# Kernel optimization log

Hardware: AMD Instinct MI355X
Metric: run time of the kernel (lower is better)

## Reference

```python
import jax, jax.numpy as jnp
import numpy as np

FLOAT_MIN = np.float32(np.finfo(np.float32).min)  # torch.finfo().min for float32
K_DIM = 64  # init kwarg, equals head dim of query/key


def setup_inputs() -> dict:
    key = jax.random.key(0)
    k1, k2, k3, k4 = jax.random.split(key, 4)
    B, Lq, Lk, D, Dv = 16, 2048, 2048, 64, 64
    return {
        "query": jax.random.normal(k1, (B, Lq, D), dtype=jnp.float32),
        "key": jax.random.normal(k2, (B, Lk, D), dtype=jnp.float32),
        "value": jax.random.normal(k3, (B, Lk, Dv), dtype=jnp.float32),
        "mask": jax.random.uniform(k4, (1, Lq, Lk), dtype=jnp.float32),
    }


def reference(query, key, value, mask):
    # scores: [B, Lq, Lk]
    scores = jnp.einsum("bqd,bkd->bqk", query, key) / jnp.sqrt(jnp.float32(K_DIM))
    # multiplicative mask -> additive log-bias, clamped at float32 min
    scores = scores + jnp.maximum(jnp.log(mask), FLOAT_MIN)
    # NOTE: source applies softmax over dim=1 (the query axis), faithfully reproduced
    attn = jax.nn.softmax(scores, axis=1)
    return jnp.einsum("bqk,bkv->bqv", attn, value)
```

## Files before the change

kernel.cpp:

```cpp
#include <hip/hip_runtime.h>
#include <cstdint>
#include <cstddef>


#define LSEQ 2048
#define DHEAD 64

typedef __bf16 v8bf __attribute__((ext_vector_type(8)));
typedef __bf16 v4bf __attribute__((ext_vector_type(4)));
typedef float v4f __attribute__((ext_vector_type(4)));

#define MFMA16(a, b, c) __builtin_amdgcn_mfma_f32_16x16x32_bf16(a, b, c, 0, 0, 0)

__device__ __forceinline__ void gl_lds16(const void* g, void* l) {
  __builtin_amdgcn_global_load_lds(
      (__attribute__((address_space(1))) void*)g,
      (__attribute__((address_space(3))) void*)l, 16, 0, 0);
}

__global__ __launch_bounds__(256) void cast_qk(const float* __restrict__ Q,
                                               const float* __restrict__ K,
                                               __bf16* __restrict__ Qb,
                                               __bf16* __restrict__ Kb,
                                               float* __restrict__ outz,
                                               float* __restrict__ Lz) {
  size_t j = (size_t)blockIdx.x * 256 + threadIdx.x;
  size_t i = j * 4;
  float4 q = *(const float4*)(Q + i);
  float4 k = *(const float4*)(K + i);
  v4bf qo = {(__bf16)(q.x * 0.125f), (__bf16)(q.y * 0.125f),
             (__bf16)(q.z * 0.125f), (__bf16)(q.w * 0.125f)};
  v4bf ko = {(__bf16)k.x, (__bf16)k.y, (__bf16)k.z, (__bf16)k.w};
  *(v4bf*)(Qb + i) = qo;
  *(v4bf*)(Kb + i) = ko;
  float4 z = {0.f, 0.f, 0.f, 0.f};
  *(float4*)(outz + i) = z;
  if (j < (size_t)16 * LSEQ) Lz[j] = 0.f;
}

__global__ __launch_bounds__(256, 4) void stats_k(const __bf16* __restrict__ Qb,
                                                  const __bf16* __restrict__ Kb,
                                                  const float* __restrict__ mask,
                                                  float* __restrict__ Lsum) {
  const int bx = blockIdx.x;
  const int b = bx >> 7;
  const int qc = (bx >> 5) & 3;
  const int k0 = (bx & 31) * 64;
  const int tid = threadIdx.x;
  const int w = tid >> 6, lane = tid & 63;
  const int quad = lane >> 4, n = lane & 15;

  __shared__ __align__(16) __bf16 Qt[2][64 * 64];
  __shared__ float psum[4][64];

#define STAGE_Q(buf, q0s)                                                        \
  {                                                                              \
    _Pragma("unroll") for (int i = 0; i < 2; ++i) {                              \
      int s = (w * 2 + i) * 64 + lane;                                           \
      int row = s >> 3, gc = (s & 7) ^ (row & 7);                                \
      gl_lds16(Qb + ((size_t)b * LSEQ + (q0s) + row) * DHEAD + gc * 8,           \
               &Qt[buf][s * 8]);                                                 \
    }                                                                            \
  }

  v8bf ak[4][2];
#pragma unroll
  for (int sub = 0; sub < 4; ++sub)
#pragma unroll
    for (int dh = 0; dh < 2; ++dh)
      ak[sub][dh] = *(const v8bf*)(Kb + ((size_t)b * LSEQ + k0 + sub * 16 + n) * DHEAD +
                                   dh * 32 + quad * 8);

  float csum[4][4];
#pragma unroll
  for (int sub = 0; sub < 4; ++sub)
#pragma unroll
    for (int r = 0; r < 4; ++r) csum[sub][r] = 0.f;

  const int qbeg = qc * 512;
  STAGE_Q(0, qbeg);
  __syncthreads();

  int cur = 0;
#pragma unroll 1
  for (int ks = 0; ks < 8; ++ks) {
    const int qs = qbeg + ks * 64;
    v4f m4[4];
#pragma unroll
    for (int sub = 0; sub < 4; ++sub)
      m4[sub] = *(const v4f*)(mask + (size_t)(qs + w * 16 + n) * LSEQ + k0 + sub * 16 +
                              quad * 4);
    if (ks < 7) STAGE_Q(cur ^ 1, qs + 64);

    const int qr = w * 16 + n;
    v8bf bq[2];
#pragma unroll
    for (int dh = 0; dh < 2; ++dh)
      bq[dh] = *(const v8bf*)&Qt[cur][qr * 64 + ((dh * 4 + quad) ^ (qr & 7)) * 8];

    __builtin_amdgcn_s_setprio(1);
#pragma unroll
    for (int sub = 0; sub < 4; ++sub) {
      v4f c = {0.f, 0.f, 0.f, 0.f};
      c = MFMA16(ak[sub][0], bq[0], c);
      c = MFMA16(ak[sub][1], bq[1], c);
#pragma unroll
      for (int r = 0; r < 4; ++r) csum[sub][r] += m4[sub][r] * __expf(c[r]);
    }
    __builtin_amdgcn_s_setprio(0);
    __syncthreads();
    cur ^= 1;
  }
#undef STAGE_Q

#pragma unroll
  for (int sub = 0; sub < 4; ++sub)
#pragma unroll
    for (int r = 0; r < 4; ++r) {
      float v = csum[sub][r];
      v += __shfl_xor(v, 1);
      v += __shfl_xor(v, 2);
      v += __shfl_xor(v, 4);
      v += __shfl_xor(v, 8);
      if (n == 0) psum[w][sub * 16 + quad * 4 + r] = v;
    }
  __syncthreads();
  if (tid < 64) {
    float s = psum[0][tid] + psum[1][tid] + psum[2][tid] + psum[3][tid];
    unsafeAtomicAdd(&Lsum[(size_t)b * LSEQ + k0 + tid], s);
  }
}

__global__ __launch_bounds__(256) void vtrans_k(const float* __restrict__ V,
                                                const float* __restrict__ Lsum,
                                                __bf16* __restrict__ Vts) {
  const int b = blockIdx.x >> 6;
  const int k0 = (blockIdx.x & 63) * 32;
  const int tid = threadIdx.x;
  __shared__ float tile[32][65];
  __shared__ float invl[32];
  if (tid < 32) invl[tid] = 1.0f / Lsum[(size_t)b * LSEQ + k0 + tid];
#pragma unroll
  for (int t = 0; t < 8; ++t) {
    int flat = t * 256 + tid;
    int k = flat >> 6, v = flat & 63;
    tile[k][v] = V[((size_t)b * LSEQ + k0 + k) * DHEAD + v];
  }
  __syncthreads();
#pragma unroll
  for (int t = 0; t < 8; ++t) {
    int flat = t * 256 + tid;
    int v = flat >> 5, k = flat & 31;
    Vts[((size_t)b * DHEAD + v) * LSEQ + k0 + k] = (__bf16)(tile[k][v] * invl[k]);
  }
}

__global__ __launch_bounds__(256, 4) void attn_k(const __bf16* __restrict__ Qb,
                                                 const __bf16* __restrict__ Kb,
                                                 const __bf16* __restrict__ Vts,
                                                 const float* __restrict__ mask,
                                                 float* __restrict__ out) {
  const int bx = blockIdx.x;
  const int b = bx >> 6;
  const int kc = (bx >> 4) & 3;
  const int q0 = (bx & 15) * 128;
  const int tid = threadIdx.x;
  const int w = tid >> 6, lane = tid & 63;
  const int quad = lane >> 4, n = lane & 15;

  __shared__ __align__(16) __bf16 Kt[64 * 64];
  __shared__ __align__(16) __bf16 Vt[64 * 64];
  __shared__ __align__(16) __bf16 Pt[128 * 64];

#define STAGE_K(kb2)                                                             \
  {                                                                              \
    _Pragma("unroll") for (int i = 0; i < 2; ++i) {                              \
      int s = (w * 2 + i) * 64 + lane;                                           \
      int row = s >> 3, gc = (s & 7) ^ (row & 7);                                \
      gl_lds16(Kb + ((size_t)b * LSEQ + (kb2) + row) * DHEAD + gc * 8,           \
               &Kt[s * 8]);                                                      \
    }                                                                            \
  }
#define STAGE_V(kb2)                                                             \
  {                                                                              \
    _Pragma("unroll") for (int i = 0; i < 2; ++i) {                              \
      int s = (w * 2 + i) * 64 + lane;                                           \
      int row = s >> 3, gc = (s & 7) ^ (row & 7);                                \
      gl_lds16(Vts + ((size_t)b * DHEAD + row) * LSEQ + (kb2) + gc * 8,          \
               &Vt[s * 8]);                                                      \
    }                                                                            \
  }

  const int qg0 = q0 + w * 32 + n;

  v8bf bq[2][2];
#pragma unroll
  for (int h = 0; h < 2; ++h)
#pragma unroll
    for (int dh = 0; dh < 2; ++dh)
      bq[h][dh] = *(const v8bf*)(Qb + ((size_t)b * LSEQ + qg0 + h * 16) * DHEAD +
                                 dh * 32 + quad * 8);

  v4f acc[2][4];
#pragma unroll
  for (int h = 0; h < 2; ++h)
#pragma unroll
    for (int vs = 0; vs < 4; ++vs) acc[h][vs] = (v4f){0.f, 0.f, 0.f, 0.f};

  const int kbeg = kc * 512;
  STAGE_K(kbeg);
  STAGE_V(kbeg);
  __syncthreads();

#pragma unroll 1
  for (int ks = 0; ks < 8; ++ks) {
    const int kb = kbeg + ks * 64;
    v4f m4[2][4];
#pragma unroll
    for (int h = 0; h < 2; ++h)
#pragma unroll
      for (int sub = 0; sub < 4; ++sub)
        m4[h][sub] = *(const v4f*)(mask + (size_t)(qg0 + h * 16) * LSEQ + kb + sub * 16 +
                                   quad * 4);

    __builtin_amdgcn_s_setprio(1);
#pragma unroll
    for (int sub = 0; sub < 4; ++sub) {
      const int kr = sub * 16 + n;
      v8bf a0 = *(const v8bf*)&Kt[kr * 64 + ((quad) ^ (kr & 7)) * 8];
      v8bf a1 = *(const v8bf*)&Kt[kr * 64 + ((4 + quad) ^ (kr & 7)) * 8];
#pragma unroll
      for (int h = 0; h < 2; ++h) {
        v4f c = {0.f, 0.f, 0.f, 0.f};
        c = MFMA16(a0, bq[h][0], c);
        c = MFMA16(a1, bq[h][1], c);
        v4bf pv;
#pragma unroll
        for (int r = 0; r < 4; ++r) pv[r] = (__bf16)(m4[h][sub][r] * __expf(c[r]));
        const int prow = w * 32 + h * 16 + n;
        *(v4bf*)((char*)Pt + prow * 128 + (((sub * 2 + (quad >> 1)) ^ (n & 7)) << 4) +
                 ((quad & 1) << 3)) = pv;
      }
    }
    __builtin_amdgcn_s_setprio(0);
    __syncthreads();
    if (ks < 7) STAGE_K(kb + 64);

    __builtin_amdgcn_s_setprio(1);
#pragma unroll
    for (int kk = 0; kk < 2; ++kk) {
      const int pr0 = w * 32 + n, pr1 = pr0 + 16;
      v8bf ap0 =
          *(const v8bf*)((char*)Pt + pr0 * 128 + (((kk * 4 + quad) ^ (n & 7)) << 4));
      v8bf ap1 =
          *(const v8bf*)((char*)Pt + pr1 * 128 + (((kk * 4 + quad) ^ (n & 7)) << 4));
#pragma unroll
      for (int vs = 0; vs < 4; ++vs) {
        const int vr = vs * 16 + n;
        v8bf bv = *(const v8bf*)&Vt[vr * 64 + ((kk * 4 + quad) ^ (vr & 7)) * 8];
        acc[0][vs] = MFMA16(ap0, bv, acc[0][vs]);
        acc[1][vs] = MFMA16(ap1, bv, acc[1][vs]);
      }
    }
    __builtin_amdgcn_s_setprio(0);
    __syncthreads();
    if (ks < 7) STAGE_V(kb + 64);
  }
#undef STAGE_K
#undef STAGE_V

#pragma unroll
  for (int h = 0; h < 2; ++h)
#pragma unroll
    for (int vs = 0; vs < 4; ++vs)
#pragma unroll
      for (int r = 0; r < 4; ++r)
        unsafeAtomicAdd(&out[((size_t)b * LSEQ + q0 + w * 32 + h * 16 + quad * 4 + r) *
                                 DHEAD +
                             vs * 16 + n],
                        acc[h][vs][r]);
}

extern "C" void kernel_launch(void* const* d_in, const int* in_sizes, int n_in,
                              void* d_out, int out_size, void* d_ws, size_t ws_size,
                              hipStream_t stream) {
  const float* Q = (const float*)d_in[0];
  const float* K = (const float*)d_in[1];
  const float* V = (const float*)d_in[2];
  const float* mask = (const float*)d_in[3];
  float* out = (float*)d_out;

  char* ws = (char*)d_ws;
  __bf16* Qb = (__bf16*)(ws);
  __bf16* Kb = (__bf16*)(ws + (4 << 20));
  __bf16* Vts = (__bf16*)(ws + (8 << 20));
  float* Lsum = (float*)(ws + (12 << 20));
  const size_t need = ((size_t)12 << 20) + (1 << 17);
  if (ws_size < need) return;

  cast_qk<<<2048, 256, 0, stream>>>(Q, K, Qb, Kb, out, Lsum);
  stats_k<<<2048, 256, 0, stream>>>(Qb, Kb, mask, Lsum);
  vtrans_k<<<1024, 256, 0, stream>>>(V, Lsum, Vts);
  attn_k<<<1024, 256, 0, stream>>>(Qb, Kb, Vts, mask, out);
}
```

Baseline: 184.3 us.

## Fuse four kernels into one cooperative persistent kernel with grid syncs

```diff
diff --git a/kernel.cpp b/kernel.cpp
--- a/kernel.cpp
+++ b/kernel.cpp
@@ -1,4 +1,5 @@
 #include <hip/hip_runtime.h>
+#include <hip/hip_cooperative_groups.h>
 #include <cstdint>
 #include <cstddef>
 
@@ -18,267 +19,260 @@
       (__attribute__((address_space(3))) void*)l, 16, 0, 0);
 }
 
-__global__ __launch_bounds__(256) void cast_qk(const float* __restrict__ Q,
-                                               const float* __restrict__ K,
-                                               __bf16* __restrict__ Qb,
-                                               __bf16* __restrict__ Kb,
-                                               float* __restrict__ outz,
-                                               float* __restrict__ Lz) {
-  size_t j = (size_t)blockIdx.x * 256 + threadIdx.x;
-  size_t i = j * 4;
-  float4 q = *(const float4*)(Q + i);
-  float4 k = *(const float4*)(K + i);
-  v4bf qo = {(__bf16)(q.x * 0.125f), (__bf16)(q.y * 0.125f),
-             (__bf16)(q.z * 0.125f), (__bf16)(q.w * 0.125f)};
-  v4bf ko = {(__bf16)k.x, (__bf16)k.y, (__bf16)k.z, (__bf16)k.w};
-  *(v4bf*)(Qb + i) = qo;
-  *(v4bf*)(Kb + i) = ko;
-  float4 z = {0.f, 0.f, 0.f, 0.f};
-  *(float4*)(outz + i) = z;
-  if (j < (size_t)16 * LSEQ) Lz[j] = 0.f;
-}
-
-__global__ __launch_bounds__(256, 4) void stats_k(const __bf16* __restrict__ Qb,
-                                                  const __bf16* __restrict__ Kb,
-                                                  const float* __restrict__ mask,
-                                                  float* __restrict__ Lsum) {
+struct StatsS {
+  __bf16 Qt[2][64 * 64];
+  __bf16 Kt[2][64 * 64];
+  float Lacc[16][64];
+};
+struct AttnS {
+  __bf16 Kt[64 * 64];
+  __bf16 Vt[64 * 64];
+  __bf16 Pt[128 * 64];
+};
+struct VtrS {
+  float tile[32][65];
+  float invl[32];
+};
+
+__global__ __launch_bounds__(256, 4) void fused_k(
+    const float* __restrict__ Q, const float* __restrict__ K,
+    const float* __restrict__ V, const float* __restrict__ mask,
+    __bf16* __restrict__ Qb, __bf16* __restrict__ Kb, __bf16* __restrict__ Vts,
+    float* __restrict__ Lsum, float* __restrict__ out, int phases) {
+  __shared__ __align__(16) union {
+    StatsS s;
+    AttnS a;
+    VtrS t;
+  } sm;
   const int bx = blockIdx.x;
-  const int b = bx >> 7;
-  const int qc = (bx >> 5) & 3;
-  const int k0 = (bx & 31) * 64;
   const int tid = threadIdx.x;
   const int w = tid >> 6, lane = tid & 63;
   const int quad = lane >> 4, n = lane & 15;
 
-  __shared__ __align__(16) __bf16 Qt[2][64 * 64];
-  __shared__ float psum[4][64];
-
-#define STAGE_Q(buf, q0s)                                                        \
+  if (phases & 1) {
+#pragma unroll
+    for (int rep = 0; rep < 2; ++rep) {
+      size_t j = (size_t)(bx * 2 + rep) * 256 + tid;
+      size_t i = j * 4;
+      float4 q = *(const float4*)(Q + i);
+      float4 k = *(const float4*)(K + i);
+      v4bf qo = {(__bf16)(q.x * 0.125f), (__bf16)(q.y * 0.125f),
+                 (__bf16)(q.z * 0.125f), (__bf16)(q.w * 0.125f)};
+      v4bf ko = {(__bf16)k.x, (__bf16)k.y, (__bf16)k.z, (__bf16)k.w};
+      *(v4bf*)(Qb + i) = qo;
+      *(v4bf*)(Kb + i) = ko;
+      float4 z = {0.f, 0.f, 0.f, 0.f};
+      *(float4*)(out + i) = z;
+    }
+    if (bx < 128) Lsum[bx * 256 + tid] = 0.f;
+  }
+  if (phases & 16) cooperative_groups::this_grid().sync();
+
+  if (phases & 2) {
+    auto& S = sm.s;
+    const int qt = bx >> 5, kt = bx & 31;
+    const int q0 = qt * 64, k0 = kt * 64;
+#pragma unroll
+    for (int t = 0; t < 4; ++t) ((float*)S.Lacc)[t * 256 + tid] = 0.f;
+    float msk[4][4];
+#pragma unroll
+    for (int sub = 0; sub < 4; ++sub)
+#pragma unroll
+      for (int r = 0; r < 4; ++r)
+        msk[sub][r] =
+            mask[(size_t)(q0 + w * 16 + quad * 4 + r) * LSEQ + k0 + sub * 16 + n];
+
+#define SSTAGE(buf, bb)                                                          \
   {                                                                              \
     _Pragma("unroll") for (int i = 0; i < 2; ++i) {                              \
       int s = (w * 2 + i) * 64 + lane;                                           \
       int row = s >> 3, gc = (s & 7) ^ (row & 7);                                \
-      gl_lds16(Qb + ((size_t)b * LSEQ + (q0s) + row) * DHEAD + gc * 8,           \
-               &Qt[buf][s * 8]);                                                 \
+      gl_lds16(Qb + ((size_t)(bb) * LSEQ + q0 + row) * DHEAD + gc * 8,           \
+               &S.Qt[buf][s * 8]);                                               \
+      gl_lds16(Kb + ((size_t)(bb) * LSEQ + k0 + row) * DHEAD + gc * 8,           \
+               &S.Kt[buf][s * 8]);                                               \
     }                                                                            \
   }
-
-  v8bf ak[4][2];
-#pragma unroll
-  for (int sub = 0; sub < 4; ++sub)
-#pragma unroll
-    for (int dh = 0; dh < 2; ++dh)
-      ak[sub][dh] = *(const v8bf*)(Kb + ((size_t)b * LSEQ + k0 + sub * 16 + n) * DHEAD +
-                                   dh * 32 + quad * 8);
-
-  float csum[4][4];
-#pragma unroll
-  for (int sub = 0; sub < 4; ++sub)
-#pragma unroll
-    for (int r = 0; r < 4; ++r) csum[sub][r] = 0.f;
-
-  const int qbeg = qc * 512;
-  STAGE_Q(0, qbeg);
-  __syncthreads();
-
-  int cur = 0;
+    SSTAGE(0, 0);
+    __syncthreads();
+
+    int cur = 0;
 #pragma unroll 1
-  for (int ks = 0; ks < 8; ++ks) {
-    const int qs = qbeg + ks * 64;
-    v4f m4[4];
-#pragma unroll
-    for (int sub = 0; sub < 4; ++sub)
-      m4[sub] = *(const v4f*)(mask + (size_t)(qs + w * 16 + n) * LSEQ + k0 + sub * 16 +
-                              quad * 4);
-    if (ks < 7) STAGE_Q(cur ^ 1, qs + 64);
-
-    const int qr = w * 16 + n;
-    v8bf bq[2];
-#pragma unroll
-    for (int dh = 0; dh < 2; ++dh)
-      bq[dh] = *(const v8bf*)&Qt[cur][qr * 64 + ((dh * 4 + quad) ^ (qr & 7)) * 8];
-
-    __builtin_amdgcn_s_setprio(1);
-#pragma unroll
-    for (int sub = 0; sub < 4; ++sub) {
-      v4f c = {0.f, 0.f, 0.f, 0.f};
-      c = MFMA16(ak[sub][0], bq[0], c);
-      c = MFMA16(ak[sub][1], bq[1], c);
-#pragma unroll
-      for (int r = 0; r < 4; ++r) csum[sub][r] += m4[sub][r] * __expf(c[r]);
-    }
-    __builtin_amdgcn_s_setprio(0);
+    for (int b = 0; b < 16; ++b) {
+      if (b < 15) SSTAGE(cur ^ 1, b + 1);
+      const int qr = w * 16 + n;
+      v8bf aq0 = *(const v8bf*)&S.Qt[cur][qr * 64 + ((quad) ^ (qr & 7)) * 8];
+      v8bf aq1 = *(const v8bf*)&S.Qt[cur][qr * 64 + ((4 + quad) ^ (qr & 7)) * 8];
+      float red[4];
+      __builtin_amdgcn_s_setprio(1);
+#pragma unroll
+      for (int sub = 0; sub < 4; ++sub) {
+        const int kr = sub * 16 + n;
+        v8bf b0 = *(const v8bf*)&S.Kt[cur][kr * 64 + ((quad) ^ (kr & 7)) * 8];
+        v8bf b1 = *(const v8bf*)&S.Kt[cur][kr * 64 + ((4 + quad) ^ (kr & 7)) * 8];
+        v4f c = {0.f, 0.f, 0.f, 0.f};
+        c = MFMA16(aq0, b0, c);
+        c = MFMA16(aq1, b1, c);
+        float v = msk[sub][0] * __expf(c[0]) + msk[sub][1] * __expf(c[1]) +
+                  msk[sub][2] * __expf(c[2]) + msk[sub][3] * __expf(c[3]);
+        v += __shfl_xor(v, 16);
+        v += __shfl_xor(v, 32);
+        red[sub] = v;
+      }
+      __builtin_amdgcn_s_setprio(0);
+      if (quad == 0) {
+#pragma unroll
+        for (int sub = 0; sub < 4; ++sub)
+          atomicAdd(&S.Lacc[b][sub * 16 + n], red[sub]);
+      }
+      __syncthreads();
+      cur ^= 1;
+    }
+#undef SSTAGE
+#pragma unroll
+    for (int p = 0; p < 4; ++p) {
+      int idx = p * 256 + tid;
+      unsafeAtomicAdd(&Lsum[(size_t)(idx >> 6) * LSEQ + k0 + (idx & 63)],
+                      ((float*)S.Lacc)[idx]);
+    }
+  }
+  if (phases & 16) cooperative_groups::this_grid().sync();
+
+  if (phases & 4) {
+    auto& T = sm.t;
+    const int b = bx >> 6;
+    const int k0v = (bx & 63) * 32;
+    if (tid < 32) T.invl[tid] = 1.0f / Lsum[(size_t)b * LSEQ + k0v + tid];
+#pragma unroll
+    for (int t = 0; t < 8; ++t) {
+      int flat = t * 256 + tid;
+      int k = flat >> 6, v = flat & 63;
+      T.tile[k][v] = V[((size_t)b * LSEQ + k0v + k) * DHEAD + v];
+    }
     __syncthreads();
-    cur ^= 1;
-  }
-#undef STAGE_Q
-
-#pragma unroll
-  for (int sub = 0; sub < 4; ++sub)
-#pragma unroll
-    for (int r = 0; r < 4; ++r) {
-      float v = csum[sub][r];
-      v += __shfl_xor(v, 1);
-      v += __shfl_xor(v, 2);
-      v += __shfl_xor(v, 4);
-      v += __shfl_xor(v, 8);
-      if (n == 0) psum[w][sub * 16 + quad * 4 + r] = v;
-    }
-  __syncthreads();
-  if (tid < 64) {
-    float s = psum[0][tid] + psum[1][tid] + psum[2][tid] + psum[3][tid];
-    unsafeAtomicAdd(&Lsum[(size_t)b * LSEQ + k0 + tid], s);
-  }
-}
-
-__global__ __launch_bounds__(256) void vtrans_k(const float* __restrict__ V,
-                                                const float* __restrict__ Lsum,
-                                                __bf16* __restrict__ Vts) {
-  const int b = blockIdx.x >> 6;
-  const int k0 = (blockIdx.x & 63) * 32;
-  const int tid = threadIdx.x;
-  __shared__ float tile[32][65];
-  __shared__ float invl[32];
-  if (tid < 32) invl[tid] = 1.0f / Lsum[(size_t)b * LSEQ + k0 + tid];
-#pragma unroll
-  for (int t = 0; t < 8; ++t) {
-    int flat = t * 256 + tid;
-    int k = flat >> 6, v = flat & 63;
-    tile[k][v] = V[((size_t)b * LSEQ + k0 + k) * DHEAD + v];
-  }
-  __syncthreads();
-#pragma unroll
-  for (int t = 0; t < 8; ++t) {
-    int flat = t * 256 + tid;
-    int v = flat >> 5, k = flat & 31;
-    Vts[((size_t)b * DHEAD + v) * LSEQ + k0 + k] = (__bf16)(tile[k][v] * invl[k]);
-  }
-}
-
-__global__ __launch_bounds__(256, 4) void attn_k(const __bf16* __restrict__ Qb,
-                                                 const __bf16* __restrict__ Kb,
-                                                 const __bf16* __restrict__ Vts,
-                                                 const float* __restrict__ mask,
-                                                 float* __restrict__ out) {
-  const int bx = blockIdx.x;
-  const int b = bx >> 6;
-  const int kc = (bx >> 4) & 3;
-  const int q0 = (bx & 15) * 128;
-  const int tid = threadIdx.x;
-  const int w = tid >> 6, lane = tid & 63;
-  const int quad = lane >> 4, n = lane & 15;
-
-  __shared__ __align__(16) __bf16 Kt[64 * 64];
-  __shared__ __align__(16) __bf16 Vt[64 * 64];
-  __shared__ __align__(16) __bf16 Pt[128 * 64];
-
-#define STAGE_K(kb2)                                                             \
+#pragma unroll
+    for (int t = 0; t < 8; ++t) {
+      int flat = t * 256 + tid;
+      int v = flat >> 5, k = flat & 31;
+      Vts[((size_t)b * DHEAD + v) * LSEQ + k0v + k] = (__bf16)(T.tile[k][v] * T.invl[k]);
+    }
+  }
+  if (phases & 16) cooperative_groups::this_grid().sync();
+
+  if (phases & 8) {
+    auto& A = sm.a;
+    const int b = bx >> 6;
+    const int kc = (bx >> 4) & 3;
+    const int q0 = (bx & 15) * 128;
+
+#define ASTAGE_K(kb2)                                                            \
   {                                                                              \
     _Pragma("unroll") for (int i = 0; i < 2; ++i) {                              \
       int s = (w * 2 + i) * 64 + lane;                                           \
       int row = s >> 3, gc = (s & 7) ^ (row & 7);                                \
       gl_lds16(Kb + ((size_t)b * LSEQ + (kb2) + row) * DHEAD + gc * 8,           \
-               &Kt[s * 8]);                                                      \
+               &A.Kt[s * 8]);                                                    \
     }                                                                            \
   }
-#define STAGE_V(kb2)                                                             \
+#define ASTAGE_V(kb2)                                                            \
   {                                                                              \
     _Pragma("unroll") for (int i = 0; i < 2; ++i) {                              \
       int s = (w * 2 + i) * 64 + lane;                                           \
       int row = s >> 3, gc = (s & 7) ^ (row & 7);                                \
       gl_lds16(Vts + ((size_t)b * DHEAD + row) * LSEQ + (kb2) + gc * 8,          \
-               &Vt[s * 8]);                                                      \
+               &A.Vt[s * 8]);                                                    \
     }                                                                            \
   }
 
-  const int qg0 = q0 + w * 32 + n;
-
-  v8bf bq[2][2];
-#pragma unroll
-  for (int h = 0; h < 2; ++h)
-#pragma unroll
-    for (int dh = 0; dh < 2; ++dh)
-      bq[h][dh] = *(const v8bf*)(Qb + ((size_t)b * LSEQ + qg0 + h * 16) * DHEAD +
-                                 dh * 32 + quad * 8);
-
-  v4f acc[2][4];
-#pragma unroll
-  for (int h = 0; h < 2; ++h)
-#pragma unroll
-    for (int vs = 0; vs < 4; ++vs) acc[h][vs] = (v4f){0.f, 0.f, 0.f, 0.f};
-
-  const int kbeg = kc * 512;
-  STAGE_K(kbeg);
-  STAGE_V(kbeg);
-  __syncthreads();
+    const int qg0 = q0 + w * 32 + n;
+
+    v8bf bq[2][2];
+#pragma unroll
+    for (int h = 0; h < 2; ++h)
+#pragma unroll
+      for (int dh = 0; dh < 2; ++dh)
+        bq[h][dh] = *(const v8bf*)(Qb + ((size_t)b * LSEQ + qg0 + h * 16) * DHEAD +
+                                   dh * 32 + quad * 8);
+
+    v4f acc[2][4];
+#pragma unroll
+    for (int h = 0; h < 2; ++h)
+#pragma unroll
+      for (int vs = 0; vs < 4; ++vs) acc[h][vs] = (v4f){0.f, 0.f, 0.f, 0.f};
+
+    const int kbeg = kc * 512;
+    ASTAGE_K(kbeg);
+    ASTAGE_V(kbeg);
+    __syncthreads();
 
 #pragma unroll 1
-  for (int ks = 0; ks < 8; ++ks) {
-    const int kb = kbeg + ks * 64;
-    v4f m4[2][4];
+    for (int ks = 0; ks < 8; ++ks) {
+      const int kb = kbeg + ks * 64;
+      v4f m4[2][4];
+#pragma unroll
+      for (int h = 0; h < 2; ++h)
+#pragma unroll
+        for (int sub = 0; sub < 4; ++sub)
+          m4[h][sub] = *(const v4f*)(mask + (size_t)(qg0 + h * 16) * LSEQ + kb +
+                                     sub * 16 + quad * 4);
+
+      __builtin_amdgcn_s_setprio(1);
+#pragma unroll
+      for (int sub = 0; sub < 4; ++sub) {
+        const int kr = sub * 16 + n;
+        v8bf a0 = *(const v8bf*)&A.Kt[kr * 64 + ((quad) ^ (kr & 7)) * 8];
+        v8bf a1 = *(const v8bf*)&A.Kt[kr * 64 + ((4 + quad) ^ (kr & 7)) * 8];
+#pragma unroll
+        for (int h = 0; h < 2; ++h) {
+          v4f c = {0.f, 0.f, 0.f, 0.f};
+          c = MFMA16(a0, bq[h][0], c);
+          c = MFMA16(a1, bq[h][1], c);
+          v4bf pv;
+#pragma unroll
+          for (int r = 0; r < 4; ++r) pv[r] = (__bf16)(m4[h][sub][r] * __expf(c[r]));
+          const int prow = w * 32 + h * 16 + n;
+          *(v4bf*)((char*)A.Pt + prow * 128 +
+                   (((sub * 2 + (quad >> 1)) ^ (n & 7)) << 4) + ((quad & 1) << 3)) = pv;
+        }
+      }
+      __builtin_amdgcn_s_setprio(0);
+      __syncthreads();
+      if (ks < 7) ASTAGE_K(kb + 64);
+
+      __builtin_amdgcn_s_setprio(1);
+#pragma unroll
+      for (int kk = 0; kk < 2; ++kk) {
+        const int pr0 = w * 32 + n, pr1 = pr0 + 16;
+        v8bf ap0 =
+            *(const v8bf*)((char*)A.Pt + pr0 * 128 + (((kk * 4 + quad) ^ (n & 7)) << 4));
+        v8bf ap1 =
+            *(const v8bf*)((char*)A.Pt + pr1 * 128 + (((kk * 4 + quad) ^ (n & 7)) << 4));
+#pragma unroll
+        for (int vs = 0; vs < 4; ++vs) {
+          const int vr = vs * 16 + n;
+          v8bf bv = *(const v8bf*)&A.Vt[vr * 64 + ((kk * 4 + quad) ^ (vr & 7)) * 8];
+          acc[0][vs] = MFMA16(ap0, bv, acc[0][vs]);
+          acc[1][vs] = MFMA16(ap1, bv, acc[1][vs]);
+        }
+      }
+      __builtin_amdgcn_s_setprio(0);
+      __syncthreads();
+      if (ks < 7) ASTAGE_V(kb + 64);
+    }
+#undef ASTAGE_K
+#undef ASTAGE_V
+
 #pragma unroll
     for (int h = 0; h < 2; ++h)
 #pragma unroll
-      for (int sub = 0; sub < 4; ++sub)
-        m4[h][sub] = *(const v4f*)(mask + (size_t)(qg0 + h * 16) * LSEQ + kb + sub * 16 +
-                                   quad * 4);
-
-    __builtin_amdgcn_s_setprio(1);
-#pragma unroll
-    for (int sub = 0; sub < 4; ++sub) {
-      const int kr = sub * 16 + n;
-      v8bf a0 = *(const v8bf*)&Kt[kr * 64 + ((quad) ^ (kr & 7)) * 8];
-      v8bf a1 = *(const v8bf*)&Kt[kr * 64 + ((4 + quad) ^ (kr & 7)) * 8];
-#pragma unroll
-      for (int h = 0; h < 2; ++h) {
-        v4f c = {0.f, 0.f, 0.f, 0.f};
-        c = MFMA16(a0, bq[h][0], c);
-        c = MFMA16(a1, bq[h][1], c);
-        v4bf pv;
-#pragma unroll
-        for (int r = 0; r < 4; ++r) pv[r] = (__bf16)(m4[h][sub][r] * __expf(c[r]));
-        const int prow = w * 32 + h * 16 + n;
-        *(v4bf*)((char*)Pt + prow * 128 + (((sub * 2 + (quad >> 1)) ^ (n & 7)) << 4) +
-                 ((quad & 1) << 3)) = pv;
-      }
-    }
-    __builtin_amdgcn_s_setprio(0);
-    __syncthreads();
-    if (ks < 7) STAGE_K(kb + 64);
-
-    __builtin_amdgcn_s_setprio(1);
-#pragma unroll
-    for (int kk = 0; kk < 2; ++kk) {
-      const int pr0 = w * 32 + n, pr1 = pr0 + 16;
-      v8bf ap0 =
-          *(const v8bf*)((char*)Pt + pr0 * 128 + (((kk * 4 + quad) ^ (n & 7)) << 4));
-      v8bf ap1 =
-          *(const v8bf*)((char*)Pt + pr1 * 128 + (((kk * 4 + quad) ^ (n & 7)) << 4));
-#pragma unroll
-      for (int vs = 0; vs < 4; ++vs) {
-        const int vr = vs * 16 + n;
-        v8bf bv = *(const v8bf*)&Vt[vr * 64 + ((kk * 4 + quad) ^ (vr & 7)) * 8];
-        acc[0][vs] = MFMA16(ap0, bv, acc[0][vs]);
-        acc[1][vs] = MFMA16(ap1, bv, acc[1][vs]);
-      }
-    }
-    __builtin_amdgcn_s_setprio(0);
-    __syncthreads();
-    if (ks < 7) STAGE_V(kb + 64);
-  }
-#undef STAGE_K
-#undef STAGE_V
-
-#pragma unroll
-  for (int h = 0; h < 2; ++h)
-#pragma unroll
-    for (int vs = 0; vs < 4; ++vs)
-#pragma unroll
-      for (int r = 0; r < 4; ++r)
-        unsafeAtomicAdd(&out[((size_t)b * LSEQ + q0 + w * 32 + h * 16 + quad * 4 + r) *
-                                 DHEAD +
-                             vs * 16 + n],
-                        acc[h][vs][r]);
+      for (int vs = 0; vs < 4; ++vs)
+#pragma unroll
+        for (int r = 0; r < 4; ++r)
+          unsafeAtomicAdd(&out[((size_t)b * LSEQ + q0 + w * 32 + h * 16 + quad * 4 + r) *
+                                   DHEAD +
+                               vs * 16 + n],
+                          acc[h][vs][r]);
+  }
 }
 
 extern "C" void kernel_launch(void* const* d_in, const int* in_sizes, int n_in,
@@ -298,8 +292,19 @@
   const size_t need = ((size_t)12 << 20) + (1 << 17);
   if (ws_size < need) return;
 
-  cast_qk<<<2048, 256, 0, stream>>>(Q, K, Qb, Kb, out, Lsum);
-  stats_k<<<2048, 256, 0, stream>>>(Qb, Kb, mask, Lsum);
-  vtrans_k<<<1024, 256, 0, stream>>>(V, Lsum, Vts);
-  attn_k<<<1024, 256, 0, stream>>>(Qb, Kb, Vts, mask, out);
+  int nb = 0;
+  hipOccupancyMaxActiveBlocksPerMultiprocessor(&nb, fused_k, 256, 0);
+  if (nb >= 4) {
+    int phases = 31;
+    void* args[] = {(void*)&Q,  (void*)&K,    (void*)&V,    (void*)&mask,
+                    (void*)&Qb, (void*)&Kb,   (void*)&Vts,  (void*)&Lsum,
+                    (void*)&out, (void*)&phases};
+    hipError_t e = hipLaunchCooperativeKernel(fused_k, dim3(1024), dim3(256), args,
+                                              (unsigned)0, stream);
+    if (e == hipSuccess) return;
+  }
+  fused_k<<<1024, 256, 0, stream>>>(Q, K, V, mask, Qb, Kb, Vts, Lsum, out, 1);
+  fused_k<<<1024, 256, 0, stream>>>(Q, K, V, mask, Qb, Kb, Vts, Lsum, out, 2);
+  fused_k<<<1024, 256, 0, stream>>>(Q, K, V, mask, Qb, Kb, Vts, Lsum, out, 4);
+  fused_k<<<1024, 256, 0, stream>>>(Q, K, V, mask, Qb, Kb, Vts, Lsum, out, 8);
 }
```

Measured after the change: 185.4 us. No clear change (+0.6%).
